# Kernel optimization log

Hardware: AMD Instinct MI355X
Metric: run time of the kernel (lower is better)

The kernel has to match this reference:

```python
import math
import jax, jax.numpy as jnp
import numpy as np

HIDDEN = 1024
NUM_HEADS = 16
NUM_QUERIES = 2
NUM_Q_HEADS = NUM_HEADS * NUM_QUERIES  # 32
HEAD_DIM = 64
Q_DIM = NUM_Q_HEADS * HEAD_DIM   # 2048
KV_DIM = NUM_HEADS * HEAD_DIM    # 1024
BATCH, SEQ = 4, 1024


def _alibi_slopes(num_heads: int) -> np.ndarray:
    # num_heads is a power of two here, so only the main branch applies
    closest_pow2 = 2 ** int(math.floor(math.log2(num_heads)))
    base = 2.0 ** (-(2.0 ** (-(math.log2(closest_pow2) - 3))))
    powers = np.arange(1, closest_pow2 + 1, dtype=np.float32)
    slopes = base ** powers
    if closest_pow2 != num_heads:
        extra_base = 2.0 ** (-(2.0 ** (-(math.log2(2 * closest_pow2) - 3))))
        extra_powers = np.arange(1, 2 * (num_heads - closest_pow2) + 1, 2, dtype=np.float32)
        slopes = np.concatenate([slopes, extra_base ** extra_powers])
    return slopes[:num_heads].astype(np.float32)

ALIBI_SLOPES = jnp.asarray(_alibi_slopes(NUM_Q_HEADS))  # (32,)


def setup_inputs() -> dict:
    key = jax.random.key(0)
    k1, k2, k3 = jax.random.split(key, 3)
    inputs = jax.random.normal(k1, (BATCH, SEQ, HIDDEN), dtype=jnp.float32)
    # match nn.Linear default init scale roughly
    W_qkv = jax.random.normal(k2, (HIDDEN, Q_DIM + 2 * KV_DIM), dtype=jnp.float32) * (1.0 / math.sqrt(HIDDEN))
    W_out = jax.random.normal(k3, (Q_DIM, HIDDEN), dtype=jnp.float32) * (1.0 / math.sqrt(Q_DIM))
    return {"inputs": inputs, "W_qkv": W_qkv, "W_out": W_out}


def reference(inputs, W_qkv, W_out):
    B, S, _ = inputs.shape
    qkv = inputs @ W_qkv                                   # [B,S,4096]
    q = qkv[..., :Q_DIM].reshape(B, S, NUM_Q_HEADS, HEAD_DIM).transpose(0, 2, 1, 3)   # [B,32,S,64]
    k = qkv[..., Q_DIM:Q_DIM + KV_DIM].reshape(B, S, NUM_HEADS, HEAD_DIM).transpose(0, 2, 1, 3)
    v = qkv[..., Q_DIM + KV_DIM:].reshape(B, S, NUM_HEADS, HEAD_DIM).transpose(0, 2, 1, 3)
    # GQA: repeat_interleave along head dim
    k = jnp.repeat(k, NUM_QUERIES, axis=1)                 # [B,32,S,64]
    v = jnp.repeat(v, NUM_QUERIES, axis=1)
    # ALiBi bias: slope_h * (kv_pos - q_pos)
    pos = jnp.arange(S)
    rel = (pos[None, :] - pos[:, None]).astype(jnp.float32)           # [S,S]
    bias = ALIBI_SLOPES[:, None, None] * rel[None, :, :]              # [32,S,S]
    scores = jnp.einsum('bhqd,bhkd->bhqk', q, k) / math.sqrt(HEAD_DIM)
    scores = scores + bias[None]
    causal = pos[:, None] >= pos[None, :]                             # [S,S]
    scores = jnp.where(causal[None, None], scores, -jnp.inf)
    attn = jax.nn.softmax(scores, axis=-1)
    out = jnp.einsum('bhqk,bhkd->bhqd', attn, v)                      # [B,32,S,64]
    out = out.transpose(0, 2, 1, 3).reshape(B, S, Q_DIM)
    return out @ W_out                                                # [B,S,HIDDEN]
```

## Files before the change

### kernel.cpp

```cpp
#include <hip/hip_runtime.h>

typedef unsigned short u16;
typedef unsigned int u32;
typedef float f32x4 __attribute__((ext_vector_type(4)));
typedef float f32x16 __attribute__((ext_vector_type(16)));
typedef __bf16 bf16x8 __attribute__((ext_vector_type(8)));
typedef short short8 __attribute__((ext_vector_type(8)));
typedef u16 u16x4 __attribute__((ext_vector_type(4)));
typedef float f32x4v __attribute__((ext_vector_type(4)));

#define DEV __device__ __forceinline__

DEV u16 f2bf(float f) {
    union { float f; unsigned u; } v; v.f = f;
    unsigned r = v.u + 0x7FFFu + ((v.u >> 16) & 1u);
    return (u16)(r >> 16);
}

DEV void gload_lds16(const u16* g, u16* l) {
    __builtin_amdgcn_global_load_lds(
        (const __attribute__((address_space(1))) void*)g,
        (__attribute__((address_space(3))) void*)l, 16, 0, 0);
}

__global__ __launch_bounds__(256) void k_cvt(const float* __restrict__ in,
                                             u16* __restrict__ out, int n4) {
    int i = blockIdx.x * 256 + threadIdx.x;
    if (i >= n4) return;
    f32x4v v = reinterpret_cast<const f32x4v*>(in)[i];
    u16x4 o;
    o.x = f2bf(v.x); o.y = f2bf(v.y); o.z = f2bf(v.z); o.w = f2bf(v.w);
    reinterpret_cast<u16x4*>(out)[i] = o;
}

__global__ __launch_bounds__(256) void k_transpose_cvt(const float* __restrict__ in,
                                                       u16* __restrict__ out,
                                                       int R, int C) {
    __shared__ float tile[32][33];
    const int c0 = blockIdx.x * 32, r0 = blockIdx.y * 32;
    const int tx = threadIdx.x & 31, ty = threadIdx.x >> 5;
#pragma unroll
    for (int i = 0; i < 32; i += 8)
        tile[ty + i][tx] = in[(size_t)(r0 + ty + i) * C + c0 + tx];
    __syncthreads();
#pragma unroll
    for (int i = 0; i < 32; i += 8)
        out[(size_t)(c0 + ty + i) * R + r0 + tx] = f2bf(tile[tx][ty + i]);
}

template <int OUTF>
__global__ __launch_bounds__(256) void k_gemm_nt(const u16* __restrict__ A,
                                                 const u16* __restrict__ Bt,
                                                 void* __restrict__ Cv,
                                                 int M, int N, int K) {
    __shared__ u16 lA[2][4096];
    __shared__ u16 lB[2][4096];
    const int t = threadIdx.x, l = t & 63, w = t >> 6;
    const int bm = blockIdx.y * 128, bn = blockIdx.x * 128;
    const int wr = w >> 1, wc = w & 1;
    const int lm = l & 15, lg = l >> 4;

    f32x4 acc[4][4] = {};

    const int nk = K >> 5;
    auto stage = [&](int buf, int kt) {
        const int k0 = kt << 5;
        const int kc = (l & 3) * 8;
        const int rsub = w * 16 + (l >> 2);
#pragma unroll
        for (int p = 0; p < 2; ++p) {
            const int row = p * 64 + rsub;
            gload_lds16(A + (size_t)(bm + row) * K + k0 + kc, &lA[buf][p * 2048 + w * 512]);
            gload_lds16(Bt + (size_t)(bn + row) * K + k0 + kc, &lB[buf][p * 2048 + w * 512]);
        }
    };

    stage(0, 0);
    __syncthreads();
    for (int kt = 0; kt < nk; ++kt) {
        const int buf = kt & 1;
        if (kt + 1 < nk) stage(buf ^ 1, kt + 1);
        bf16x8 af[4], bfr[4];
#pragma unroll
        for (int i = 0; i < 4; ++i) {
            af[i]  = *reinterpret_cast<const bf16x8*>(&lA[buf][(wr * 64 + i * 16 + lm) * 32 + lg * 8]);
            bfr[i] = *reinterpret_cast<const bf16x8*>(&lB[buf][(wc * 64 + i * 16 + lm) * 32 + lg * 8]);
        }
        __builtin_amdgcn_s_setprio(1);
#pragma unroll
        for (int mi = 0; mi < 4; ++mi)
#pragma unroll
            for (int ni = 0; ni < 4; ++ni)
                acc[mi][ni] = __builtin_amdgcn_mfma_f32_16x16x32_bf16(af[mi], bfr[ni], acc[mi][ni], 0, 0, 0);
        __builtin_amdgcn_s_setprio(0);
        __syncthreads();
    }

#pragma unroll
    for (int mi = 0; mi < 4; ++mi)
#pragma unroll
        for (int ni = 0; ni < 4; ++ni)
#pragma unroll
            for (int r = 0; r < 4; ++r) {
                const int row = bm + wr * 64 + mi * 16 + lg * 4 + r;
                const int col = bn + wc * 64 + ni * 16 + lm;
                if (OUTF)
                    reinterpret_cast<float*>(Cv)[(size_t)row * N + col] = acc[mi][ni][r];
                else
                    reinterpret_cast<u16*>(Cv)[(size_t)row * N + col] = f2bf(acc[mi][ni][r]);
            }
}

template <int OUTF>
__global__ __launch_bounds__(512, 2) void k_gemm256(const u16* __restrict__ A,
                                                    const u16* __restrict__ Bt,
                                                    void* __restrict__ Cv,
                                                    int M, int N, int K) {
    __shared__ u16 lA[4][8192];
    __shared__ u16 lB[4][8192];
    const int t = threadIdx.x, l = t & 63, w = t >> 6;
    int bid;
    {
        const int nwg = gridDim.x, cpx = nwg >> 3, b0 = blockIdx.x;
        bid = (b0 & 7) * cpx + (b0 >> 3);
    }
    const int nbx = N >> 8;
    const int bm = (bid / nbx) << 8, bn = (bid % nbx) << 8;
    const int wm = w >> 2, wn = w & 3;
    const int lm = l & 15, lg = l >> 4;

    f32x4 acc[8][4] = {};
    const int nk = K >> 5;

    auto stage = [&](int kt) {
        const int buf = kt & 3;
        const int k0 = kt << 5;
#pragma unroll
        for (int p = 0; p < 2; ++p) {
            const int idx = p * 512 + t;
            const int row = idx >> 2, ch = idx & 3;
            const int sc = (ch ^ ((row ^ (row >> 2)) & 3)) << 3;
            gload_lds16(A + (size_t)(bm + row) * K + k0 + sc, &lA[buf][p * 4096 + w * 512]);
            gload_lds16(Bt + (size_t)(bn + row) * K + k0 + sc, &lB[buf][p * 4096 + w * 512]);
        }
    };

    stage(0);
    if (nk > 1) stage(1);
    if (nk > 2) stage(2);

    for (int kt = 0; kt < nk; ++kt) {
        const int buf = kt & 3;
        const int rem = nk - 1 - kt;
        if (rem >= 2)      asm volatile("s_waitcnt vmcnt(8)" ::: "memory");
        else if (rem == 1) asm volatile("s_waitcnt vmcnt(4)" ::: "memory");
        else               asm volatile("s_waitcnt vmcnt(0)" ::: "memory");
        __builtin_amdgcn_s_barrier();
        __builtin_amdgcn_sched_barrier(0);
        if (kt + 3 < nk) stage(kt + 3);

        bf16x8 af[8], bf_[4];
#pragma unroll
        for (int i = 0; i < 8; ++i) {
            const int row = wm * 128 + i * 16 + lm;
            af[i] = *reinterpret_cast<const bf16x8*>(
                &lA[buf][row * 32 + ((lg ^ ((row ^ (row >> 2)) & 3)) << 3)]);
        }
#pragma unroll
        for (int i = 0; i < 4; ++i) {
            const int row = wn * 64 + i * 16 + lm;
            bf_[i] = *reinterpret_cast<const bf16x8*>(
                &lB[buf][row * 32 + ((lg ^ ((row ^ (row >> 2)) & 3)) << 3)]);
        }
        __builtin_amdgcn_s_setprio(1);
#pragma unroll
        for (int mi = 0; mi < 8; ++mi)
#pragma unroll
            for (int ni = 0; ni < 4; ++ni)
                acc[mi][ni] = __builtin_amdgcn_mfma_f32_16x16x32_bf16(af[mi], bf_[ni], acc[mi][ni], 0, 0, 0);
        __builtin_amdgcn_s_setprio(0);
    }

#pragma unroll
    for (int mi = 0; mi < 8; ++mi)
#pragma unroll
        for (int ni = 0; ni < 4; ++ni)
#pragma unroll
            for (int r = 0; r < 4; ++r) {
                const int row = bm + wm * 128 + mi * 16 + lg * 4 + r;
                const int col = bn + wn * 64 + ni * 16 + lm;
                if (OUTF)
                    reinterpret_cast<float*>(Cv)[(size_t)row * N + col] = acc[mi][ni][r];
                else
                    reinterpret_cast<u16*>(Cv)[(size_t)row * N + col] = f2bf(acc[mi][ni][r]);
            }
}

__global__ __launch_bounds__(512, 4) void k_attn(const u16* __restrict__ qkv,
                                                 u16* __restrict__ AO) {
    __shared__ u16 lK[2][4096];
    __shared__ u16 lVT[2][4096];
    __shared__ float lSc[8][32];

    const int t = threadIdx.x, l = t & 63, w = t >> 6;
    const int lo5 = l & 31, hi = l >> 5;
    const int fid = blockIdx.x;
    const int half = fid >> 8, idx = fid & 255;
    const int j = idx & 1, hb = idx >> 1;
    const int hq = hb >> 2, b = hb & 3;
    const int qb = half ? (j ? 2 : 0) : (j ? 1 : 3);
    const int hkv = hq >> 1;
    const float L2E = 1.44269504088896f;
    const float slope2 = exp2f(-0.25f * (float)(hq + 1)) * L2E;
    const float scale2 = 0.125f * L2E;
    const size_t RS = 4096;
    const u16* Qg = qkv + (size_t)(b * 1024 + qb * 256) * RS + hq * 64;
    const u16* Kg = qkv + (size_t)(b * 1024) * RS + 2048 + hkv * 64;
    const u16* Vg = qkv + (size_t)(b * 1024) * RS + 3072 + hkv * 64;

    const int q = qb * 256 + w * 32 + lo5;

    bf16x8 qfr[4];
#pragma unroll
    for (int ks = 0; ks < 4; ++ks)
        qfr[ks] = *reinterpret_cast<const bf16x8*>(
            Qg + (size_t)(w * 32 + lo5) * RS + ks * 16 + hi * 8);

    f32x16 acc0 = {}, acc1 = {};
    float m_ = -3.0e38f, l_ = 0.f;

    const int nt = (qb + 1) * 4;
    const int kbd = (qb * 256 + w * 32 + 31) >> 6;

    auto stageK = [&](int buf, int kb) {
        const int row = t >> 3;
        const int ch = (t & 7) ^ (row & 7);
        gload_lds16(Kg + (size_t)(kb * 64 + row) * RS + ch * 8, &lK[buf][w * 512]);
    };
    const int kvp = t >> 3, vd0 = (t & 7) * 8;
    auto loadV = [&](int kb, short8& a, short8& b2) {
        a  = *reinterpret_cast<const short8*>(Vg + (size_t)(kb * 64 + kvp * 2) * RS + vd0);
        b2 = *reinterpret_cast<const short8*>(Vg + (size_t)(kb * 64 + kvp * 2 + 1) * RS + vd0);
    };
    auto writeV = [&](int buf, short8 a, short8 b2) {
        const int kv0 = kvp * 2;
        const int kvs0 = (kv0 & ~12) | ((kv0 & 4) << 1) | ((kv0 & 8) >> 1);
#pragma unroll
        for (int jj = 0; jj < 8; ++jj) {
            const int d = vd0 + jj;
            const int key = (d ^ (d >> 3)) & 7;
            const u32 val = (u32)(u16)a[jj] | ((u32)(u16)b2[jj] << 16);
            *reinterpret_cast<u32*>(
                &lVT[buf][d * 64 + (((kvs0 >> 3) ^ key) & 7) * 8 + (kvs0 & 7)]) = val;
        }
    };

    short8 vA, vB;
    stageK(0, 0);
    if (t < 256) { loadV(0, vA, vB); writeV(0, vA, vB); }
    __syncthreads();

    for (int kb = 0; kb < nt; ++kb) {
        const int buf = kb & 1;
        const bool pre = (kb + 1 < nt);
        if (pre) {
            stageK(buf ^ 1, kb + 1);
            if (t < 256) loadV(kb + 1, vA, vB);
        }

        if (kb <= kbd) {
            f32x16 sc0 = {}, sc1 = {};
#pragma unroll
            for (int ks = 0; ks < 4; ++ks) {
                const int csw = ((ks * 2 + hi) ^ (lo5 & 7)) * 8;
                bf16x8 ka0 = *reinterpret_cast<const bf16x8*>(&lK[buf][lo5 * 64 + csw]);
                bf16x8 ka1 = *reinterpret_cast<const bf16x8*>(&lK[buf][(32 + lo5) * 64 + csw]);
                __builtin_amdgcn_s_setprio(1);
                sc0 = __builtin_amdgcn_mfma_f32_32x32x16_bf16(ka0, qfr[ks], sc0, 0, 0, 0);
                sc1 = __builtin_amdgcn_mfma_f32_32x32x16_bf16(ka1, qfr[ks], sc1, 0, 0, 0);
                __builtin_amdgcn_s_setprio(0);
            }
            float s[32];
            const float b0 = slope2 * (float)(kb * 64 + 4 * hi - q);
            const float b1 = slope2 * (float)(kb * 64 + 32 + 4 * hi - q);
#pragma unroll
            for (int r = 0; r < 16; ++r) {
                const int Cr = (r & 3) + 8 * (r >> 2);
                s[r]      = fmaf(sc0[r], scale2, fmaf(slope2, (float)Cr, b0));
                s[16 + r] = fmaf(sc1[r], scale2, fmaf(slope2, (float)Cr, b1));
            }
            if (kb == kbd) {
                const int qr0 = q - kb * 64 - 4 * hi;
#pragma unroll
                for (int r = 0; r < 16; ++r) {
                    const int Cr = (r & 3) + 8 * (r >> 2);
                    if (Cr > qr0)      s[r]      = -3.0e38f;
                    if (Cr + 32 > qr0) s[16 + r] = -3.0e38f;
                }
            }
            float tm[16];
#pragma unroll
            for (int i = 0; i < 16; ++i) tm[i] = fmaxf(s[i], s[16 + i]);
#pragma unroll
            for (int i = 0; i < 8; ++i) tm[i] = fmaxf(tm[i], tm[8 + i]);
#pragma unroll
            for (int i = 0; i < 4; ++i) tm[i] = fmaxf(tm[i], tm[4 + i]);
            float mx = fmaxf(fmaxf(tm[0], tm[1]), fmaxf(tm[2], tm[3]));
            mx = fmaxf(mx, __shfl_xor(mx, 32));
            const float mnew = fmaxf(m_, mx);
            const float sclf = exp2f(m_ - mnew);
            m_ = mnew;
#pragma unroll
            for (int i = 0; i < 32; ++i) s[i] = exp2f(s[i] - mnew);
            float ts[16];
#pragma unroll
            for (int i = 0; i < 16; ++i) ts[i] = s[i] + s[16 + i];
#pragma unroll
            for (int i = 0; i < 8; ++i) ts[i] += ts[8 + i];
#pragma unroll
            for (int i = 0; i < 4; ++i) ts[i] += ts[4 + i];
            float sum = (ts[0] + ts[1]) + (ts[2] + ts[3]);
            sum += __shfl_xor(sum, 32);
            l_ = l_ * sclf + sum;
            lSc[w][lo5] = sclf;
            asm volatile("s_waitcnt lgkmcnt(0)" ::: "memory");
            float rs_[16];
#pragma unroll
            for (int r = 0; r < 16; ++r) {
                const int Cr = (r & 3) + 8 * (r >> 2);
                rs_[r] = lSc[w][Cr + 4 * hi];
            }
#pragma unroll
            for (int r = 0; r < 16; ++r) { acc0[r] *= rs_[r]; acc1[r] *= rs_[r]; }
            u32 pw[16];
#pragma unroll
            for (int s4 = 0; s4 < 4; ++s4) {
                const int off = (s4 >> 1) * 16 + (s4 & 1) * 8;
#pragma unroll
                for (int jj = 0; jj < 4; ++jj) {
                    u32 o;
                    asm("v_cvt_pk_bf16_f32 %0, %1, %2"
                        : "=v"(o) : "v"(s[off + 2 * jj]), "v"(s[off + 2 * jj + 1]));
                    pw[s4 * 4 + jj] = o;
                }
            }
            const int key0 = (lo5 ^ (lo5 >> 3)) & 7;
            const int key1 = ((32 + lo5) ^ ((32 + lo5) >> 3)) & 7;
#pragma unroll
            for (int s4 = 0; s4 < 4; ++s4) {
                bf16x8 pa;
                u32* paw = reinterpret_cast<u32*>(&pa);
                paw[0] = pw[s4 * 4 + 0]; paw[1] = pw[s4 * 4 + 1];
                paw[2] = pw[s4 * 4 + 2]; paw[3] = pw[s4 * 4 + 3];
                const int cl = s4 * 2 + hi;
                bf16x8 va0 = *reinterpret_cast<const bf16x8*>(&lVT[buf][lo5 * 64 + ((cl ^ key0) & 7) * 8]);
                bf16x8 va1 = *reinterpret_cast<const bf16x8*>(&lVT[buf][(32 + lo5) * 64 + ((cl ^ key1) & 7) * 8]);
                __builtin_amdgcn_s_setprio(1);
                acc0 = __builtin_amdgcn_mfma_f32_32x32x16_bf16(pa, va0, acc0, 0, 0, 0);
                acc1 = __builtin_amdgcn_mfma_f32_32x32x16_bf16(pa, va1, acc1, 0, 0, 0);
                __builtin_amdgcn_s_setprio(0);
            }
        }

        if (pre && t < 256) writeV(buf ^ 1, vA, vB);
        __syncthreads();
    }

    lSc[w][lo5] = 1.0f / l_;
    asm volatile("s_waitcnt lgkmcnt(0)" ::: "memory");
    float rl[16];
#pragma unroll
    for (int r = 0; r < 16; ++r) {
        const int Cr = (r & 3) + 8 * (r >> 2);
        rl[r] = lSc[w][Cr + 4 * hi];
    }
    u16* AOp = AO + (size_t)(b * 1024 + qb * 256 + w * 32) * 2048 + hq * 64;
#pragma unroll
    for (int r = 0; r < 16; ++r) {
        const int Cr = (r & 3) + 8 * (r >> 2);
        const size_t rowoff = (size_t)(Cr + 4 * hi) * 2048;
        AOp[rowoff + lo5]      = f2bf(acc0[r] * rl[r]);
        AOp[rowoff + 32 + lo5] = f2bf(acc1[r] * rl[r]);
    }
}

extern "C" void kernel_launch(void* const* d_in, const int* in_sizes, int n_in,
                              void* d_out, int out_size, void* d_ws, size_t ws_size,
                              hipStream_t stream) {
    const float* X    = (const float*)d_in[0];
    const float* Wqkv = (const float*)d_in[1];
    const float* Wout = (const float*)d_in[2];
    float* out = (float*)d_out;

    char* ws = (char*)d_ws;
    u16* Xb    = (u16*)(ws);
    u16* WqkvT = (u16*)(ws + (size_t)(8  << 20));
    u16* WoutT = (u16*)(ws + (size_t)(16 << 20));
    u16* QKV   = (u16*)(ws + (size_t)(20 << 20));
    u16* AO    = (u16*)(ws + (size_t)(52 << 20));

    k_cvt<<<4096, 256, 0, stream>>>(X, Xb, (4096 * 1024) / 4);
    k_transpose_cvt<<<dim3(128, 32), 256, 0, stream>>>(Wqkv, WqkvT, 1024, 4096);
    k_transpose_cvt<<<dim3(32, 64), 256, 0, stream>>>(Wout, WoutT, 2048, 1024);

    k_gemm256<0><<<dim3(256), 512, 0, stream>>>(Xb, WqkvT, QKV, 4096, 4096, 1024);

    k_attn<<<dim3(512), 512, 0, stream>>>(QKV, AO);

    k_gemm_nt<1><<<dim3(8, 32), 256, 0, stream>>>(AO, WoutT, out, 4096, 1024, 2048);
}
```

Before: 266.5 us.

## Triple-buffer K/V tiles with manual vmcnt waits and XCD-aware block mapping

The attention kernel's K and transposed-V LDS buffers go from two stages to three, so loads for tile kb+2 are issued while tile kb is computed. The end-of-iteration __syncthreads is replaced by explicit s_waitcnt vmcnt/lgkmcnt counts and raw s_barrier, which lets later loads stay in flight across the barrier. Block indices are also remapped so that the Q heads and query blocks sharing one KV head and batch land on the same XCD, which should improve L2 reuse of K/V. In exchange, LDS use rises and occupancy may fall, and the hand-counted vmcnt values depend on the exact number of outstanding loads.

New measurement: 294.1 us. 1.1x slower.

```diff
diff --git a/kernel.cpp b/kernel.cpp
--- a/kernel.cpp
+++ b/kernel.cpp
@@ -198,18 +198,19 @@
 
 __global__ __launch_bounds__(512, 4) void k_attn(const u16* __restrict__ qkv,
                                                  u16* __restrict__ AO) {
-    __shared__ u16 lK[2][4096];
-    __shared__ u16 lVT[2][4096];
+    __shared__ u16 lK[3][4096];
+    __shared__ u16 lVT[3][4096];
     __shared__ float lSc[8][32];
 
     const int t = threadIdx.x, l = t & 63, w = t >> 6;
     const int lo5 = l & 31, hi = l >> 5;
     const int fid = blockIdx.x;
-    const int half = fid >> 8, idx = fid & 255;
-    const int j = idx & 1, hb = idx >> 1;
-    const int hq = hb >> 2, b = hb & 3;
-    const int qb = half ? (j ? 2 : 0) : (j ? 1 : 3);
-    const int hkv = hq >> 1;
+    const int xcd = fid & 7, within = fid >> 3;
+    const int gh = within >> 3, s_ = within & 7;
+    const int g = gh * 8 + xcd;
+    const int hkv = g >> 2, b = g & 3;
+    const int hq = hkv * 2 + (s_ & 1);
+    const int qb = (int)(((gh < 4) ? 0x0213u : 0x3120u) >> ((s_ >> 1) * 4)) & 7;
     const float L2E = 1.44269504088896f;
     const float slope2 = exp2f(-0.25f * (float)(hq + 1)) * L2E;
     const float scale2 = 0.125f * L2E;
@@ -255,17 +256,35 @@
         }
     };
 
-    short8 vA, vB;
+    short8 vA0, vB0, vA1, vB1;
+
+    if (t < 256) loadV(0, vA0, vB0);
     stageK(0, 0);
-    if (t < 256) { loadV(0, vA, vB); writeV(0, vA, vB); }
-    __syncthreads();
-
+    if (t < 256) loadV(1, vA1, vB1);
+    stageK(1, 1);
+    if (t < 256) {
+        asm volatile("s_waitcnt vmcnt(4)" ::: "memory");
+        writeV(0, vA0, vB0);
+        asm volatile("s_waitcnt vmcnt(3) lgkmcnt(0)" ::: "memory");
+    } else {
+        asm volatile("s_waitcnt vmcnt(1)" ::: "memory");
+    }
+    __builtin_amdgcn_s_barrier();
+    __builtin_amdgcn_sched_barrier(0);
+
+    int b0 = 0;
     for (int kb = 0; kb < nt; ++kb) {
-        const int buf = kb & 1;
-        const bool pre = (kb + 1 < nt);
-        if (pre) {
-            stageK(buf ^ 1, kb + 1);
-            if (t < 256) loadV(kb + 1, vA, vB);
+        const int b1 = (b0 == 2) ? 0 : b0 + 1;
+        const int b2_ = (b1 == 2) ? 0 : b1 + 1;
+        const bool pre2 = (kb + 2 < nt);
+        const bool pre1 = (kb + 1 < nt);
+
+        if (pre2) {
+            if (t < 256) {
+                if ((kb & 1) == 0) loadV(kb + 2, vA0, vB0);
+                else               loadV(kb + 2, vA1, vB1);
+            }
+            stageK(b2_, kb + 2);
         }
 
         if (kb <= kbd) {
@@ -273,21 +292,21 @@
 #pragma unroll
             for (int ks = 0; ks < 4; ++ks) {
                 const int csw = ((ks * 2 + hi) ^ (lo5 & 7)) * 8;
-                bf16x8 ka0 = *reinterpret_cast<const bf16x8*>(&lK[buf][lo5 * 64 + csw]);
-                bf16x8 ka1 = *reinterpret_cast<const bf16x8*>(&lK[buf][(32 + lo5) * 64 + csw]);
+                bf16x8 ka0 = *reinterpret_cast<const bf16x8*>(&lK[b0][lo5 * 64 + csw]);
+                bf16x8 ka1 = *reinterpret_cast<const bf16x8*>(&lK[b0][(32 + lo5) * 64 + csw]);
                 __builtin_amdgcn_s_setprio(1);
                 sc0 = __builtin_amdgcn_mfma_f32_32x32x16_bf16(ka0, qfr[ks], sc0, 0, 0, 0);
                 sc1 = __builtin_amdgcn_mfma_f32_32x32x16_bf16(ka1, qfr[ks], sc1, 0, 0, 0);
                 __builtin_amdgcn_s_setprio(0);
             }
             float s[32];
-            const float b0 = slope2 * (float)(kb * 64 + 4 * hi - q);
-            const float b1 = slope2 * (float)(kb * 64 + 32 + 4 * hi - q);
+            const float bb0 = slope2 * (float)(kb * 64 + 4 * hi - q);
+            const float bb1 = slope2 * (float)(kb * 64 + 32 + 4 * hi - q);
 #pragma unroll
             for (int r = 0; r < 16; ++r) {
                 const int Cr = (r & 3) + 8 * (r >> 2);
-                s[r]      = fmaf(sc0[r], scale2, fmaf(slope2, (float)Cr, b0));
-                s[16 + r] = fmaf(sc1[r], scale2, fmaf(slope2, (float)Cr, b1));
+                s[r]      = fmaf(sc0[r], scale2, fmaf(slope2, (float)Cr, bb0));
+                s[16 + r] = fmaf(sc1[r], scale2, fmaf(slope2, (float)Cr, bb1));
             }
             if (kb == kbd) {
                 const int qr0 = q - kb * 64 - 4 * hi;
@@ -353,8 +372,8 @@
                 paw[0] = pw[s4 * 4 + 0]; paw[1] = pw[s4 * 4 + 1];
                 paw[2] = pw[s4 * 4 + 2]; paw[3] = pw[s4 * 4 + 3];
                 const int cl = s4 * 2 + hi;
-                bf16x8 va0 = *reinterpret_cast<const bf16x8*>(&lVT[buf][lo5 * 64 + ((cl ^ key0) & 7) * 8]);
-                bf16x8 va1 = *reinterpret_cast<const bf16x8*>(&lVT[buf][(32 + lo5) * 64 + ((cl ^ key1) & 7) * 8]);
+                bf16x8 va0 = *reinterpret_cast<const bf16x8*>(&lVT[b0][lo5 * 64 + ((cl ^ key0) & 7) * 8]);
+                bf16x8 va1 = *reinterpret_cast<const bf16x8*>(&lVT[b0][(32 + lo5) * 64 + ((cl ^ key1) & 7) * 8]);
                 __builtin_amdgcn_s_setprio(1);
                 acc0 = __builtin_amdgcn_mfma_f32_32x32x16_bf16(pa, va0, acc0, 0, 0, 0);
                 acc1 = __builtin_amdgcn_mfma_f32_32x32x16_bf16(pa, va1, acc1, 0, 0, 0);
@@ -362,8 +381,22 @@
             }
         }
 
-        if (pre && t < 256) writeV(buf ^ 1, vA, vB);
-        __syncthreads();
+        if (pre1) {
+            if (t < 256) {
+                if (pre2) asm volatile("s_waitcnt vmcnt(4)" ::: "memory");
+                else      asm volatile("s_waitcnt vmcnt(1)" ::: "memory");
+                if ((kb & 1) == 0) writeV(b1, vA1, vB1);
+                else               writeV(b1, vA0, vB0);
+                if (pre2) asm volatile("s_waitcnt vmcnt(3) lgkmcnt(0)" ::: "memory");
+                else      asm volatile("s_waitcnt vmcnt(0) lgkmcnt(0)" ::: "memory");
+            } else {
+                if (pre2) asm volatile("s_waitcnt vmcnt(1)" ::: "memory");
+                else      asm volatile("s_waitcnt vmcnt(0)" ::: "memory");
+            }
+            __builtin_amdgcn_s_barrier();
+            __builtin_amdgcn_sched_barrier(0);
+        }
+        b0 = b1;
     }
 
     lSc[w][lo5] = 1.0f / l_;
```
